# Kernel optimization log

Hardware: AMD Instinct MI355X
Metric: run time of the kernel (lower is better)

Reference implementation:

```python
import jax, jax.numpy as jnp
import numpy as np

B, S, D = 4, 4096, 1024
ROT = 4          # rotation_dim (quaternion)
MAX_SEQ = 4096   # max_seq_len
EPS = 1e-5


def setup_inputs() -> dict:
    key = jax.random.key(0)
    k_x, = jax.random.split(key, 1)
    x = jax.random.normal(k_x, (B, S, D), dtype=jnp.float32)
    # Learned parameters (torch inits: eye, ones, LN gamma=1 beta=0)
    rotation_matrix = jnp.eye(ROT, dtype=jnp.float32)
    frequency_kernel = jnp.ones((MAX_SEQ,), dtype=jnp.float32)
    ln_gamma = jnp.ones((D,), dtype=jnp.float32)
    ln_beta = jnp.zeros((D,), dtype=jnp.float32)
    return {"x": x, "rotation_matrix": rotation_matrix,
            "frequency_kernel": frequency_kernel,
            "ln_gamma": ln_gamma, "ln_beta": ln_beta}


def reference(x, rotation_matrix, frequency_kernel, ln_gamma, ln_beta):
    b, s, d = x.shape
    quat_dim = d // ROT
    # (b, s, quat_dim, 4)
    x_quat = x.reshape(b, s, quat_dim, ROT)
    # FFT along sequence axis, multiply by (real) learnable frequency kernel
    x_freq = jnp.fft.fft(x_quat, axis=1)
    kernel = frequency_kernel[:s].reshape(1, s, 1, 1)
    filtered_time = jnp.fft.ifft(x_freq * kernel, axis=1).real.astype(x.dtype)
    # Small 4x4 quaternion rotation applied to the last axis
    rotated = jnp.einsum('bstq,oq->bsto', filtered_time, rotation_matrix)
    out = rotated.reshape(b, s, d)
    # LayerNorm over the feature dim
    mean = jnp.mean(out, axis=-1, keepdims=True)
    var = jnp.var(out, axis=-1, keepdims=True)
    out = (out - mean) * jax.lax.rsqrt(var + EPS) * ln_gamma + ln_beta
    return out
```

## Files before the change

kernel.cpp:

```cpp
#include <hip/hip_runtime.h>
#include <hip/hip_bf16.h>
#include <hip/hip_fp16.h>

#define NB 4
#define NS 4096
#define ND 1024
#define LN_EPS 1e-5f

__device__ __forceinline__ int pad(int i) { return i + (i >> 4); }

__device__ __forceinline__ float2 cadd(float2 a, float2 b) { return make_float2(a.x + b.x, a.y + b.y); }
__device__ __forceinline__ float2 csub(float2 a, float2 b) { return make_float2(a.x - b.x, a.y - b.y); }
__device__ __forceinline__ float2 cmul(float2 a, float2 b) {
  return make_float2(a.x * b.x - a.y * b.y, a.x * b.y + a.y * b.x);
}
__device__ __forceinline__ float2 cmulc(float2 a, float2 b) {
  return make_float2(a.x * b.x + a.y * b.y, a.y * b.x - a.x * b.y);
}
__device__ __forceinline__ unsigned int pkh(float2 v) {
  __half2 h = __floats2half2_rn(v.x, v.y);
  return *reinterpret_cast<unsigned int*>(&h);
}
__device__ __forceinline__ float2 uph(unsigned int u) {
  __half2 h = *reinterpret_cast<__half2*>(&u);
  return __half22float2(h);
}

__device__ __forceinline__ int rev12(int p) {
  return ((p & 15) << 8) | (p & 240) | (p >> 8);
}

template<int S>
__device__ __forceinline__ void dft16(float2* x) {
  const float C1 = 0.9238795325112867f, S1 = 0.3826834323650898f, RT = 0.7071067811865476f;
  const float WC[10] = {1.f, C1, RT, S1, 0.f, -S1, -RT, -C1, -1.f, -C1};
  const float WS[10] = {0.f, S1, RT, C1, 1.f, C1,  RT,  S1,  0.f, -S1};
  #pragma unroll
  for (int m0 = 0; m0 < 4; ++m0) {
    float2 a = x[m0], b = x[m0 + 4], c = x[m0 + 8], d = x[m0 + 12];
    float2 t0 = cadd(a, c), t1 = csub(a, c), t2 = cadd(b, d), t3 = csub(b, d);
    float2 t3i = (S < 0) ? make_float2(t3.y, -t3.x) : make_float2(-t3.y, t3.x);
    x[m0]      = cadd(t0, t2);
    x[m0 + 4]  = cadd(t1, t3i);
    x[m0 + 8]  = csub(t0, t2);
    x[m0 + 12] = csub(t1, t3i);
  }
  #pragma unroll
  for (int r0 = 1; r0 < 4; ++r0)
    #pragma unroll
    for (int m0 = 1; m0 < 4; ++m0) {
      const int k = m0 * r0;
      const float2 w = make_float2(WC[k], (S < 0) ? -WS[k] : WS[k]);
      x[m0 + 4 * r0] = cmul(x[m0 + 4 * r0], w);
    }
  float2 y[16];
  #pragma unroll
  for (int r0 = 0; r0 < 4; ++r0) {
    float2 a = x[4 * r0], b = x[4 * r0 + 1], c = x[4 * r0 + 2], d = x[4 * r0 + 3];
    float2 t0 = cadd(a, c), t1 = csub(a, c), t2 = cadd(b, d), t3 = csub(b, d);
    float2 t3i = (S < 0) ? make_float2(t3.y, -t3.x) : make_float2(-t3.y, t3.x);
    y[r0]      = cadd(t0, t2);
    y[r0 + 4]  = cadd(t1, t3i);
    y[r0 + 8]  = csub(t0, t2);
    y[r0 + 12] = csub(t1, t3i);
  }
  #pragma unroll
  for (int i = 0; i < 16; ++i) x[i] = y[i];
}

__global__ void kprep(const float* __restrict__ fk, float* __restrict__ fkp,
                      float2* __restrict__ TwA, float2* __restrict__ TwC) {
  const int p = blockIdx.x * 256 + threadIdx.x;
  fkp[p] = fk[rev12(p)] * (1.0f / 4096.0f);
  const float TPON = 1.5339807878856412e-3f;
  if (p < 256) {
    const int a = p >> 4, r = p & 15;
    float sn, cs;
    __sincosf((float)(a * r) * (TPON * 16.f), &sn, &cs);
    TwA[p] = make_float2(cs, -sn);
    __sincosf((float)(a * r) * TPON, &sn, &cs);
    TwC[p] = make_float2(cs, -sn);
  }
}

__global__ __launch_bounds__(256) void ktransF(const float* __restrict__ x,
                                               float* __restrict__ xT) {
  __shared__ float tile[64][65];
  const int b = blockIdx.z;
  const int s0 = blockIdx.x * 64;
  const int d0 = blockIdx.y * 64;
  const int t = threadIdx.x;
  const float* xb = x + (size_t)b * NS * ND;
  #pragma unroll
  for (int p = 0; p < 4; ++p) {
    int r = (t >> 4) + p * 16;
    int c = (t & 15) * 4;
    float4 v = *reinterpret_cast<const float4*>(xb + (size_t)(s0 + r) * ND + (d0 + c));
    tile[r][c] = v.x; tile[r][c + 1] = v.y; tile[r][c + 2] = v.z; tile[r][c + 3] = v.w;
  }
  __syncthreads();
  float* xTb = xT + (size_t)b * ND * NS;
  #pragma unroll
  for (int p = 0; p < 4; ++p) {
    int dr = (t >> 4) + p * 16;
    int sc = (t & 15) * 4;
    float4 o;
    o.x = tile[sc + 0][dr]; o.y = tile[sc + 1][dr];
    o.z = tile[sc + 2][dr]; o.w = tile[sc + 3][dr];
    *reinterpret_cast<float4*>(xTb + (size_t)(d0 + dr) * NS + (s0 + sc)) = o;
  }
}

__global__ __launch_bounds__(512, 4) void kfft(float* __restrict__ xT,
                                               const float* __restrict__ fkp,
                                               const float2* __restrict__ TwAg,
                                               const float2* __restrict__ TwCg,
                                               const float* __restrict__ R,
                                               float* __restrict__ ssum,
                                               float* __restrict__ ssq) {
  extern __shared__ unsigned char smem[];
  unsigned int* zdyn = (unsigned int*)smem;
  float2* twl = (float2*)(smem + 34816);
  const int t = threadIdx.x;
  const int h = t >> 8;
  const int tt = t & 255;
  const int q = blockIdx.x;
  const int b = blockIdx.y;
  float* base = xT + ((size_t)b * ND + (size_t)q * 4) * NS;
  float* rowA = base + (size_t)(2 * h) * NS;
  float* rowB = base + (size_t)(2 * h + 1) * NS;
  unsigned int* zz = zdyn + (size_t)h * 4352;
  const int ta = tt >> 4, tc = tt & 15;
  float2 x[16];

  twl[t] = (t < 256) ? TwAg[t] : TwCg[t - 256];

  #pragma unroll
  for (int m = 0; m < 16; ++m)
    x[m] = make_float2(rowA[tt + 256 * m], rowB[tt + 256 * m]);
  dft16<-1>(x);
  __syncthreads();
  zz[pad(tt)] = pkh(x[0]);
  #pragma unroll
  for (int r = 1; r < 16; ++r) {
    float2 tw = cmul(twl[r * 16 + ta], twl[256 + r * 16 + tc]);
    zz[pad(tt + 256 * r)] = pkh(cmul(x[r], tw));
  }
  __syncthreads();
  {
    const int bs = 256 * (tt >> 4) + (tt & 15);
    const int j = tt & 15;
    #pragma unroll
    for (int m = 0; m < 16; ++m) x[m] = uph(zz[pad(bs + 16 * m)]);
    dft16<-1>(x);
    zz[pad(bs)] = pkh(x[0]);
    #pragma unroll
    for (int r = 1; r < 16; ++r) zz[pad(bs + 16 * r)] = pkh(cmul(x[r], twl[r * 16 + j]));
  }
  __syncthreads();
  {
    const int bs = 16 * tt;
    #pragma unroll
    for (int m = 0; m < 16; ++m) x[m] = uph(zz[pad(bs + m)]);
    dft16<-1>(x);
    #pragma unroll
    for (int r4 = 0; r4 < 4; ++r4) {
      float4 kv = *reinterpret_cast<const float4*>(fkp + bs + 4 * r4);
      x[4 * r4 + 0].x *= kv.x; x[4 * r4 + 0].y *= kv.x;
      x[4 * r4 + 1].x *= kv.y; x[4 * r4 + 1].y *= kv.y;
      x[4 * r4 + 2].x *= kv.z; x[4 * r4 + 2].y *= kv.z;
      x[4 * r4 + 3].x *= kv.w; x[4 * r4 + 3].y *= kv.w;
    }
    dft16<1>(x);
    #pragma unroll
    for (int r = 0; r < 16; ++r) zz[pad(bs + r)] = pkh(x[r]);
  }
  __syncthreads();
  {
    const int bs = 256 * (tt >> 4) + (tt & 15);
    const int j = tt & 15;
    x[0] = uph(zz[pad(bs)]);
    #pragma unroll
    for (int m = 1; m < 16; ++m) x[m] = cmulc(uph(zz[pad(bs + 16 * m)]), twl[m * 16 + j]);
    dft16<1>(x);
    #pragma unroll
    for (int r = 0; r < 16; ++r) zz[pad(bs + 16 * r)] = pkh(x[r]);
  }
  __syncthreads();
  {
    x[0] = uph(zz[pad(tt)]);
    #pragma unroll
    for (int m = 1; m < 16; ++m)
      x[m] = cmulc(cmulc(uph(zz[pad(tt + 256 * m)]), twl[m * 16 + ta]), twl[256 + m * 16 + tc]);
    dft16<1>(x);
    #pragma unroll
    for (int r = 0; r < 16; ++r) zz[pad(tt + 256 * r)] = pkh(x[r]);
  }
  __syncthreads();
  const float r00 = R[0],  r01 = R[1],  r02 = R[2],  r03 = R[3];
  const float r10 = R[4],  r11 = R[5],  r12 = R[6],  r13 = R[7];
  const float r20 = R[8],  r21 = R[9],  r22 = R[10], r23 = R[11];
  const float r30 = R[12], r31 = R[13], r32 = R[14], r33 = R[15];
  #pragma unroll
  for (int k = 0; k < 8; ++k) {
    const int s = t + 512 * k;
    float2 v0 = uph(zdyn[pad(s)]);
    float2 v1 = uph(zdyn[4352 + pad(s)]);
    float c0 = v0.x, c1 = v0.y, c2 = v1.x, c3 = v1.y;
    float o0 = r00 * c0 + r01 * c1 + r02 * c2 + r03 * c3;
    float o1 = r10 * c0 + r11 * c1 + r12 * c2 + r13 * c3;
    float o2 = r20 * c0 + r21 * c1 + r22 * c2 + r23 * c3;
    float o3 = r30 * c0 + r31 * c1 + r32 * c2 + r33 * c3;
    base[s] = o0;
    base[NS + s] = o1;
    base[2 * NS + s] = o2;
    base[3 * NS + s] = o3;
    atomicAdd(&ssum[b * NS + s], o0 + o1 + o2 + o3);
    atomicAdd(&ssq[b * NS + s], o0 * o0 + o1 * o1 + o2 * o2 + o3 * o3);
  }
}

__global__ __launch_bounds__(256) void kapply(const float* __restrict__ xT,
                                              const float* __restrict__ ssum,
                                              const float* __restrict__ ssq,
                                              const float* __restrict__ gam,
                                              const float* __restrict__ bet,
                                              float* __restrict__ out) {
  __shared__ float tile[64][65];
  const int b = blockIdx.z;
  const int s0 = blockIdx.x * 64;
  const int d0 = blockIdx.y * 64;
  const int t = threadIdx.x;
  const float* src = xT + ((size_t)b * ND + d0) * NS + s0;
  #pragma unroll
  for (int p = 0; p < 4; ++p) {
    int r = (t >> 4) + p * 16;
    int c = (t & 15) * 4;
    float4 v = *reinterpret_cast<const float4*>(src + (size_t)r * NS + c);
    tile[r][c] = v.x; tile[r][c + 1] = v.y; tile[r][c + 2] = v.z; tile[r][c + 3] = v.w;
  }
  __syncthreads();
  float* dst = out + ((size_t)b * NS + s0) * ND + d0;
  #pragma unroll
  for (int p = 0; p < 4; ++p) {
    int sr = (t >> 4) + p * 16;
    int s = s0 + sr;
    float mean = ssum[b * NS + s] * (1.0f / ND);
    float var = ssq[b * NS + s] * (1.0f / ND) - mean * mean;
    float inv = rsqrtf(var + LN_EPS);
    int dc = (t & 15) * 4;
    float4 g4 = *reinterpret_cast<const float4*>(gam + d0 + dc);
    float4 b4 = *reinterpret_cast<const float4*>(bet + d0 + dc);
    float4 o;
    o.x = (tile[dc + 0][sr] - mean) * inv * g4.x + b4.x;
    o.y = (tile[dc + 1][sr] - mean) * inv * g4.y + b4.y;
    o.z = (tile[dc + 2][sr] - mean) * inv * g4.z + b4.z;
    o.w = (tile[dc + 3][sr] - mean) * inv * g4.w + b4.w;
    *reinterpret_cast<float4*>(dst + (size_t)sr * ND + dc) = o;
  }
}

extern "C" void kernel_launch(void* const* d_in, const int* in_sizes, int n_in,
                              void* d_out, int out_size, void* d_ws, size_t ws_size,
                              hipStream_t stream) {
  const float* x  = (const float*)d_in[0];
  const float* R  = (const float*)d_in[1];
  const float* fk = (const float*)d_in[2];
  const float* gm = (const float*)d_in[3];
  const float* bt = (const float*)d_in[4];
  float* out = (float*)d_out;

  char* ws = (char*)d_ws;
  float*  xT   = (float*)ws;
  float*  ssum = (float*)(ws + (size_t)NB * ND * NS * 4);
  float*  ssq  = ssum + NB * NS;
  float*  fkp  = ssq + NB * NS;
  float2* TwA  = (float2*)(fkp + NS);
  float2* TwC  = TwA + 256;

  (void)hipFuncSetAttribute((const void*)kfft,
                            hipFuncAttributeMaxDynamicSharedMemorySize, 38912);

  kprep<<<16, 256, 0, stream>>>(fk, fkp, TwA, TwC);
  (void)hipMemsetAsync(ssum, 0, (size_t)NB * NS * 2 * sizeof(float), stream);
  ktransF<<<dim3(NS / 64, ND / 64, NB), 256, 0, stream>>>(x, xT);
  kfft<<<dim3(ND / 4, NB), 512, 38912, stream>>>(xT, fkp, TwA, TwC, R, ssum, ssq);
  kapply<<<dim3(NS / 64, ND / 64, NB), 256, 0, stream>>>(xT, ssum, ssq, gm, bt, out);
}
```

Measured before the change: 116.4 us.

## Keep FFT shared-memory staging in fp32 and compute LN stats in separate pass

Shared-memory staging of FFT intermediates changes from packed fp16 to full float2, which doubles dynamic LDS per block to about 72KB. The per-element atomicAdd accumulation of LayerNorm sum and sum-of-squares is removed from the FFT kernel. A new kstats2 kernel instead reads the transposed buffer and reduces over D per sequence position, so the memset is no longer needed. This trades atomic contention and fp16 rounding error for an extra full read of the 64MB intermediate and lower FFT occupancy from the larger LDS footprint.

New measurement: 107.5 us. 7.7% less time.

```diff
diff --git a/kernel.cpp b/kernel.cpp
--- a/kernel.cpp
+++ b/kernel.cpp
@@ -1,6 +1,5 @@
 #include <hip/hip_runtime.h>
 #include <hip/hip_bf16.h>
-#include <hip/hip_fp16.h>
 
 #define NB 4
 #define NS 4096
@@ -16,14 +15,6 @@
 }
 __device__ __forceinline__ float2 cmulc(float2 a, float2 b) {
   return make_float2(a.x * b.x + a.y * b.y, a.y * b.x - a.x * b.y);
-}
-__device__ __forceinline__ unsigned int pkh(float2 v) {
-  __half2 h = __floats2half2_rn(v.x, v.y);
-  return *reinterpret_cast<unsigned int*>(&h);
-}
-__device__ __forceinline__ float2 uph(unsigned int u) {
-  __half2 h = *reinterpret_cast<__half2*>(&u);
-  return __half22float2(h);
 }
 
 __device__ __forceinline__ int rev12(int p) {
@@ -115,12 +106,10 @@
                                                const float* __restrict__ fkp,
                                                const float2* __restrict__ TwAg,
                                                const float2* __restrict__ TwCg,
-                                               const float* __restrict__ R,
-                                               float* __restrict__ ssum,
-                                               float* __restrict__ ssq) {
+                                               const float* __restrict__ R) {
   extern __shared__ unsigned char smem[];
-  unsigned int* zdyn = (unsigned int*)smem;
-  float2* twl = (float2*)(smem + 34816);
+  float2* zdyn = (float2*)smem;
+  float2* twl = (float2*)(smem + 69632);
   const int t = threadIdx.x;
   const int h = t >> 8;
   const int tt = t & 255;
@@ -129,7 +118,7 @@
   float* base = xT + ((size_t)b * ND + (size_t)q * 4) * NS;
   float* rowA = base + (size_t)(2 * h) * NS;
   float* rowB = base + (size_t)(2 * h + 1) * NS;
-  unsigned int* zz = zdyn + (size_t)h * 4352;
+  float2* zz = zdyn + (size_t)h * 4352;
   const int ta = tt >> 4, tc = tt & 15;
   float2 x[16];
 
@@ -140,28 +129,28 @@
     x[m] = make_float2(rowA[tt + 256 * m], rowB[tt + 256 * m]);
   dft16<-1>(x);
   __syncthreads();
-  zz[pad(tt)] = pkh(x[0]);
+  zz[pad(tt)] = x[0];
   #pragma unroll
   for (int r = 1; r < 16; ++r) {
     float2 tw = cmul(twl[r * 16 + ta], twl[256 + r * 16 + tc]);
-    zz[pad(tt + 256 * r)] = pkh(cmul(x[r], tw));
+    zz[pad(tt + 256 * r)] = cmul(x[r], tw);
   }
   __syncthreads();
   {
     const int bs = 256 * (tt >> 4) + (tt & 15);
     const int j = tt & 15;
     #pragma unroll
-    for (int m = 0; m < 16; ++m) x[m] = uph(zz[pad(bs + 16 * m)]);
+    for (int m = 0; m < 16; ++m) x[m] = zz[pad(bs + 16 * m)];
     dft16<-1>(x);
-    zz[pad(bs)] = pkh(x[0]);
-    #pragma unroll
-    for (int r = 1; r < 16; ++r) zz[pad(bs + 16 * r)] = pkh(cmul(x[r], twl[r * 16 + j]));
+    zz[pad(bs)] = x[0];
+    #pragma unroll
+    for (int r = 1; r < 16; ++r) zz[pad(bs + 16 * r)] = cmul(x[r], twl[r * 16 + j]);
   }
   __syncthreads();
   {
     const int bs = 16 * tt;
     #pragma unroll
-    for (int m = 0; m < 16; ++m) x[m] = uph(zz[pad(bs + m)]);
+    for (int m = 0; m < 16; ++m) x[m] = zz[pad(bs + m)];
     dft16<-1>(x);
     #pragma unroll
     for (int r4 = 0; r4 < 4; ++r4) {
@@ -173,28 +162,28 @@
     }
     dft16<1>(x);
     #pragma unroll
-    for (int r = 0; r < 16; ++r) zz[pad(bs + r)] = pkh(x[r]);
+    for (int r = 0; r < 16; ++r) zz[pad(bs + r)] = x[r];
   }
   __syncthreads();
   {
     const int bs = 256 * (tt >> 4) + (tt & 15);
     const int j = tt & 15;
-    x[0] = uph(zz[pad(bs)]);
-    #pragma unroll
-    for (int m = 1; m < 16; ++m) x[m] = cmulc(uph(zz[pad(bs + 16 * m)]), twl[m * 16 + j]);
+    x[0] = zz[pad(bs)];
+    #pragma unroll
+    for (int m = 1; m < 16; ++m) x[m] = cmulc(zz[pad(bs + 16 * m)], twl[m * 16 + j]);
     dft16<1>(x);
     #pragma unroll
-    for (int r = 0; r < 16; ++r) zz[pad(bs + 16 * r)] = pkh(x[r]);
+    for (int r = 0; r < 16; ++r) zz[pad(bs + 16 * r)] = x[r];
   }
   __syncthreads();
   {
-    x[0] = uph(zz[pad(tt)]);
+    x[0] = zz[pad(tt)];
     #pragma unroll
     for (int m = 1; m < 16; ++m)
-      x[m] = cmulc(cmulc(uph(zz[pad(tt + 256 * m)]), twl[m * 16 + ta]), twl[256 + m * 16 + tc]);
+      x[m] = cmulc(cmulc(zz[pad(tt + 256 * m)], twl[m * 16 + ta]), twl[256 + m * 16 + tc]);
     dft16<1>(x);
     #pragma unroll
-    for (int r = 0; r < 16; ++r) zz[pad(tt + 256 * r)] = pkh(x[r]);
+    for (int r = 0; r < 16; ++r) zz[pad(tt + 256 * r)] = x[r];
   }
   __syncthreads();
   const float r00 = R[0],  r01 = R[1],  r02 = R[2],  r03 = R[3];
@@ -204,19 +193,42 @@
   #pragma unroll
   for (int k = 0; k < 8; ++k) {
     const int s = t + 512 * k;
-    float2 v0 = uph(zdyn[pad(s)]);
-    float2 v1 = uph(zdyn[4352 + pad(s)]);
+    float2 v0 = zdyn[pad(s)];
+    float2 v1 = zdyn[4352 + pad(s)];
     float c0 = v0.x, c1 = v0.y, c2 = v1.x, c3 = v1.y;
-    float o0 = r00 * c0 + r01 * c1 + r02 * c2 + r03 * c3;
-    float o1 = r10 * c0 + r11 * c1 + r12 * c2 + r13 * c3;
-    float o2 = r20 * c0 + r21 * c1 + r22 * c2 + r23 * c3;
-    float o3 = r30 * c0 + r31 * c1 + r32 * c2 + r33 * c3;
-    base[s] = o0;
-    base[NS + s] = o1;
-    base[2 * NS + s] = o2;
-    base[3 * NS + s] = o3;
-    atomicAdd(&ssum[b * NS + s], o0 + o1 + o2 + o3);
-    atomicAdd(&ssq[b * NS + s], o0 * o0 + o1 * o1 + o2 * o2 + o3 * o3);
+    base[s]          = r00 * c0 + r01 * c1 + r02 * c2 + r03 * c3;
+    base[NS + s]     = r10 * c0 + r11 * c1 + r12 * c2 + r13 * c3;
+    base[2 * NS + s] = r20 * c0 + r21 * c1 + r22 * c2 + r23 * c3;
+    base[3 * NS + s] = r30 * c0 + r31 * c1 + r32 * c2 + r33 * c3;
+  }
+}
+
+__global__ __launch_bounds__(256) void kstats2(const float* __restrict__ xT,
+                                               float* __restrict__ ssum,
+                                               float* __restrict__ ssq) {
+  const int b = blockIdx.y;
+  const int s0 = blockIdx.x * 64;
+  const int w = threadIdx.x >> 6;
+  const int l = threadIdx.x & 63;
+  const float* src = xT + (size_t)b * ND * NS + s0 + l;
+  float a0 = 0, q0 = 0, a1 = 0, q1 = 0, a2 = 0, q2 = 0, a3 = 0, q3 = 0;
+  for (int d = w * 4; d < ND; d += 16) {
+    float v0 = src[(size_t)(d + 0) * NS];
+    float v1 = src[(size_t)(d + 1) * NS];
+    float v2 = src[(size_t)(d + 2) * NS];
+    float v3 = src[(size_t)(d + 3) * NS];
+    a0 += v0; q0 += v0 * v0;
+    a1 += v1; q1 += v1 * v1;
+    a2 += v2; q2 += v2 * v2;
+    a3 += v3; q3 += v3 * v3;
+  }
+  __shared__ float rs[4][64], rq[4][64];
+  rs[w][l] = (a0 + a1) + (a2 + a3);
+  rq[w][l] = (q0 + q1) + (q2 + q3);
+  __syncthreads();
+  if (w == 0) {
+    ssum[b * NS + s0 + l] = (rs[0][l] + rs[1][l]) + (rs[2][l] + rs[3][l]);
+    ssq[b * NS + s0 + l]  = (rq[0][l] + rq[1][l]) + (rq[2][l] + rq[3][l]);
   }
 }
 
@@ -279,11 +291,11 @@
   float2* TwC  = TwA + 256;
 
   (void)hipFuncSetAttribute((const void*)kfft,
-                            hipFuncAttributeMaxDynamicSharedMemorySize, 38912);
+                            hipFuncAttributeMaxDynamicSharedMemorySize, 73728);
 
   kprep<<<16, 256, 0, stream>>>(fk, fkp, TwA, TwC);
-  (void)hipMemsetAsync(ssum, 0, (size_t)NB * NS * 2 * sizeof(float), stream);
   ktransF<<<dim3(NS / 64, ND / 64, NB), 256, 0, stream>>>(x, xT);
-  kfft<<<dim3(ND / 4, NB), 512, 38912, stream>>>(xT, fkp, TwA, TwC, R, ssum, ssq);
+  kfft<<<dim3(ND / 4, NB), 512, 73728, stream>>>(xT, fkp, TwA, TwC, R);
+  kstats2<<<dim3(NS / 64, NB), 256, 0, stream>>>(xT, ssum, ssq);
   kapply<<<dim3(NS / 64, ND / 64, NB), 256, 0, stream>>>(xT, ssum, ssq, gm, bt, out);
 }
```
